# Kernel tuning notes

Measured on AMD Instinct MI355X. Metric: run time of the kernel, lower is better.

The kernel has to match this reference:

```python
import jax, jax.numpy as jnp
import numpy as np

S, B, D = 1024, 32, 1024

def setup_inputs() -> dict:
    key = jax.random.key(0)
    k1, k2, k3, k4, k5 = jax.random.split(key, 5)
    x = jax.random.normal(k1, (S, B, D), dtype=jnp.float32)
    layer_input = jax.random.normal(k2, (S, B, D), dtype=jnp.float32)
    position_embedding = jax.random.normal(k3, (S, B, D), dtype=jnp.float32)
    # pad indicator == 1 (True); random pads, ~half the positions
    encoder_mask = jax.random.randint(k4, (B, S), 0, 2).astype(bool)
    W = jax.random.normal(k5, (D, 1), dtype=jnp.float32) * (1.0 / np.sqrt(D))
    b = jnp.zeros((1,), dtype=jnp.float32)
    return {"x": x, "layer_input": layer_input,
            "position_embedding": position_embedding,
            "encoder_mask": encoder_mask, "W": W, "b": b}

def reference(x, layer_input, position_embedding, encoder_mask, W, b):
    s, bsz, d = x.shape
    valid = (~encoder_mask).astype(x.dtype)            # (B, S)
    sentence_length = valid.sum(axis=-1)               # (B,)
    langtok_index = s - sentence_length                # (B,)
    # predicted soft position in [0, sentence_length]
    pred = jax.nn.sigmoid(x @ W + b)[..., 0]           # (S, B)
    pred = pred * sentence_length[None, :]             # (S, B)
    # absolute positions shifted by language-token offset
    all_pos = jnp.arange(s, dtype=x.dtype)[:, None] - langtok_index[None, :]  # (S, B)
    # distances[i, b, j] = pred[i, b] - all_pos[j, b]
    dist = pred[:, :, None] - all_pos.T[None, :, :]    # (S, B, S)
    prob = 1.0 / (dist * dist + 0.001)                 # reciprocal squared distance
    prob = prob * valid[None, :, :]                    # zero out pads along j
    prob = prob / prob.sum(axis=-1, keepdims=True)     # normalize over source positions
    # weighted sum of position embeddings: (S,B,S) x (S,B,D) -> (S,B,D)
    out = jnp.einsum('ibj,jbd->ibd', prob, position_embedding)
    out = out * valid.T[:, :, None]                    # zero out pad rows
    return out
```

## Files before the change

### kernel.cpp

```cpp
#include <hip/hip_runtime.h>


#define S_ 1024
#define B_ 32
#define D_ 1024

typedef unsigned short us;
typedef __attribute__((ext_vector_type(4))) unsigned short us4;
typedef __attribute__((ext_vector_type(4))) float f4;
typedef __attribute__((ext_vector_type(8))) short short8;

__device__ __forceinline__ float bf2f(us u){
  unsigned v = ((unsigned)u) << 16;
  float f;
  __builtin_memcpy(&f, &v, 4);
  return f;
}
__device__ __forceinline__ us f2bf(float f){
  unsigned v;
  __builtin_memcpy(&v, &f, 4);
  v = v + 0x7fffu + ((v >> 16) & 1u);
  return (us)(v >> 16);
}

__device__ __forceinline__ void gll16(const void* g, void* l){
  __builtin_amdgcn_global_load_lds(
      (const __attribute__((address_space(1))) void*)g,
      (__attribute__((address_space(3))) void*)l,
      16, 0, 0);
}

__global__ __launch_bounds__(256) void prep_k(const unsigned char* __restrict__ mask,
                                              float* __restrict__ valid,
                                              float* __restrict__ slen,
                                              float* __restrict__ ltok)
{
  const int b = blockIdx.x;
  const int t = threadIdx.x;
  __shared__ int flags[5];
  __shared__ int red[256];
  if (t < 5) flags[t] = 0;
  __syncthreads();
  for (int k = 0; k < 32; ++k){
    int p = t * 32 + k;
    unsigned v = mask[p];
    if (v){
      atomicOr(&flags[p & 3], 1);
      if (v > 1u) atomicOr(&flags[4], 1);
    }
  }
  __syncthreads();
  int fmt;
  int any123 = flags[1] | flags[2] | flags[3];
  if (!flags[4]) fmt = any123 ? 0 : 1;
  else           fmt = (flags[0] | flags[1]) ? 2 : 3;

  int cnt = 0;
#pragma unroll
  for (int q = 0; q < 4; ++q){
    int j = t + q * 256;
    size_t idx = (size_t)b * S_ + j;
    unsigned mv;
    if (fmt == 0)      mv = mask[idx];
    else if (fmt == 1) mv = ((const unsigned int*)mask)[idx];
    else if (fmt == 2) mv = ((const unsigned short*)mask)[idx];
    else               mv = ((const unsigned int*)mask)[idx] & 0x7fffffffu;
    valid[idx] = mv ? 0.0f : 1.0f;
    cnt += mv ? 0 : 1;
  }
  red[t] = cnt;
  __syncthreads();
  for (int s = 128; s > 0; s >>= 1){
    if (t < s) red[t] += red[t + s];
    __syncthreads();
  }
  if (t == 0){
    float cn = (float)red[0];
    slen[b] = cn;
    ltok[b] = (float)S_ - cn;
  }
}

__device__ __forceinline__ void rowk_body(int blk, const float* __restrict__ x,
                                          const float* __restrict__ Wp,
                                          const float* __restrict__ bp,
                                          const float* __restrict__ valid,
                                          const float* __restrict__ slen,
                                          const float* __restrict__ ltok,
                                          us* __restrict__ P,
                                          float* __restrict__ rs,
                                          float* __restrict__ c_arr,
                                          bool writeP)
{
  const int wid  = threadIdx.x >> 6;
  const int lane = threadIdx.x & 63;
  const int row  = blk * 4 + wid;
  const int b = row & (B_ - 1);
  const int i = row >> 5;

  const float4* xr = (const float4*)(x + (size_t)row * D_);
  const float4* wr = (const float4*)Wp;
  float acc = 0.f;
#pragma unroll
  for (int q = 0; q < 4; ++q){
    float4 xv = xr[q * 64 + lane];
    float4 wv = wr[q * 64 + lane];
    acc += xv.x * wv.x + xv.y * wv.y + xv.z * wv.z + xv.w * wv.w;
  }
#pragma unroll
  for (int off = 32; off > 0; off >>= 1) acc += __shfl_xor(acc, off);

  float z   = acc + bp[0];
  float sig = 1.f / (1.f + expf(-z));
  float c   = sig * slen[b] + ltok[b];

  const float4* vr = (const float4*)(valid + (size_t)b * S_);
  us4* Pr = (us4*)(P + ((size_t)b * S_ + i) * S_);
  float wsum = 0.f;
#pragma unroll
  for (int q = 0; q < 4; ++q){
    int idx = q * 64 + lane;
    float4 vv = vr[idx];
    float j0 = (float)(idx * 4);
    float d0 = c - j0;
    float d1 = c - (j0 + 1.f);
    float d2 = c - (j0 + 2.f);
    float d3 = c - (j0 + 3.f);
    us p0 = f2bf(vv.x / (d0 * d0 + 1e-3f));
    us p1 = f2bf(vv.y / (d1 * d1 + 1e-3f));
    us p2 = f2bf(vv.z / (d2 * d2 + 1e-3f));
    us p3 = f2bf(vv.w / (d3 * d3 + 1e-3f));
    if (writeP){
      us4 pv; pv.x = p0; pv.y = p1; pv.z = p2; pv.w = p3;
      Pr[idx] = pv;
    }
    wsum += bf2f(p0) + bf2f(p1) + bf2f(p2) + bf2f(p3);
  }
#pragma unroll
  for (int off = 32; off > 0; off >>= 1) wsum += __shfl_xor(wsum, off);

  if (lane == 0){
    float vi = valid[(size_t)b * S_ + i];
    rs[(size_t)b * S_ + i] = (vi != 0.f) ? (vi / wsum) : 0.f;
    c_arr[(size_t)b * S_ + i] = c;
  }
}

__device__ __forceinline__ void transp_body(int j0, int d0, int b,
                                            const float* __restrict__ pe,
                                            us* __restrict__ Etr,
                                            us* tile )
{
  const int t  = threadIdx.x;
  const int rr = t >> 4, cc = t & 15;
#pragma unroll
  for (int q = 0; q < 4; ++q){
    int j = q * 16 + rr;
    float4 v = *(const float4*)(pe + ((size_t)(j0 + j) * B_ + b) * D_ + d0 + cc * 4);
    us4 tv; tv.x = f2bf(v.x); tv.y = f2bf(v.y); tv.z = f2bf(v.z); tv.w = f2bf(v.w);
    *(us4*)&tile[j * 68 + cc * 4] = tv;
  }
  __syncthreads();
#pragma unroll
  for (int q = 0; q < 4; ++q){
    int d = q * 16 + rr;
    us4 v;
    v.x = tile[(cc * 4 + 0) * 68 + d];
    v.y = tile[(cc * 4 + 1) * 68 + d];
    v.z = tile[(cc * 4 + 2) * 68 + d];
    v.w = tile[(cc * 4 + 3) * 68 + d];
    *(us4*)(Etr + ((size_t)b * D_ + d0 + d) * S_ + j0 + cc * 4) = v;
  }
}

__global__ __launch_bounds__(256) void mid_k(const float* __restrict__ x,
                                             const float* __restrict__ Wp,
                                             const float* __restrict__ bp,
                                             const float* __restrict__ valid,
                                             const float* __restrict__ slen,
                                             const float* __restrict__ ltok,
                                             us* __restrict__ P,
                                             float* __restrict__ rs,
                                             float* __restrict__ c_arr,
                                             const float* __restrict__ pe,
                                             us* __restrict__ Etr)
{
  __shared__ us tile[64 * 68];
  const int bid = blockIdx.x;
  if (bid < (S_ * B_ / 4)){
    rowk_body(bid, x, Wp, bp, valid, slen, ltok, P, rs, c_arr, true);
  } else {
    int id2 = bid - (S_ * B_ / 4);
    int jt = id2 & 15;
    int dt = (id2 >> 4) & 15;
    int b  = id2 >> 8;
    transp_body(jt * 64, dt * 64, b, pe, Etr, tile);
  }
}

__global__ __launch_bounds__(512, 2) void gemm_k(const us* __restrict__ P,
                                                 const us* __restrict__ Etr,
                                                 const float* __restrict__ rs,
                                                 float* __restrict__ out)
{
  const int bid = blockIdx.x;
  const int xcd = bid & 7;
  const int s   = bid >> 3;
  const int b   = xcd * 4 + (s >> 4);
  const int t16 = s & 15;
  const int i0  = (t16 >> 2) * 256;
  const int n0  = (t16 & 3) * 256;

  const int tid  = threadIdx.x;
  const int wid  = tid >> 6;
  const int lane = tid & 63;
  const int wm = wid >> 2, wn = wid & 3;
  const int ml = lane & 15, quad = lane >> 4;

  __shared__ __align__(16) us lds[2][4][8192];

  const us* gsrc[4];
  {
    int p = tid;
    int r = p >> 2;
    int c = (p & 3) ^ ((r >> 1) & 3);
    const us* arow = P   + ((size_t)b * S_ + (i0 + r)) * S_;
    const us* brow = Etr + ((size_t)b * D_ + (n0 + r)) * S_;
    gsrc[0] = arow + c * 8;
    gsrc[1] = arow + 32 + c * 8;
    gsrc[2] = brow + c * 8;
    gsrc[3] = brow + 32 + c * 8;
  }
  const int dst0 = wid * 64 * 8;

  int aoff[8], boff[4];
#pragma unroll
  for (int mt = 0; mt < 8; ++mt){
    int r = wm * 128 + mt * 16 + ml;
    aoff[mt] = r * 32 + ((quad ^ ((r >> 1) & 3)) * 8);
  }
#pragma unroll
  for (int nt = 0; nt < 4; ++nt){
    int r = wn * 64 + nt * 16 + ml;
    boff[nt] = r * 32 + ((quad ^ ((r >> 1) & 3)) * 8);
  }

  f4 acc[8][4];
#pragma unroll
  for (int mt = 0; mt < 8; ++mt)
#pragma unroll
    for (int nt = 0; nt < 4; ++nt){
      f4 z = {0.0f, 0.0f, 0.0f, 0.0f};
      acc[mt][nt] = z;
    }

  auto STAGE = [&](int buf, int h, int kt){
    const us* g = gsrc[h] + kt * 64;
    us* l = &lds[buf][h][dst0];
    gll16(g,                 l);
    gll16(g + 128 * S_,      l + 4096);
  };

  STAGE(0, 0, 0); STAGE(0, 2, 0);
  STAGE(0, 1, 0); STAGE(0, 3, 0);
  asm volatile("s_waitcnt vmcnt(4)" ::: "memory");
  __builtin_amdgcn_s_barrier();
  asm volatile("" ::: "memory");

#pragma unroll 1
  for (int kt = 0; kt < 16; ++kt){
    const int buf = kt & 1, nb = buf ^ 1;
    const int ktn = (kt < 15) ? (kt + 1) : 0;
    const us* A0 = lds[buf][0];
    const us* A1 = lds[buf][1];
    const us* B0 = lds[buf][2];
    const us* B1 = lds[buf][3];
    short8 av[4], av2[4], bv[4];

#pragma unroll
    for (int mt = 0; mt < 4; ++mt) av[mt] = *(const short8*)&A0[aoff[mt]];
#pragma unroll
    for (int nt = 0; nt < 4; ++nt) bv[nt] = *(const short8*)&B0[boff[nt]];
    STAGE(nb, 0, ktn);
    __builtin_amdgcn_s_setprio(1);
#pragma unroll
    for (int mt = 0; mt < 4; ++mt)
#pragma unroll
      for (int nt = 0; nt < 4; ++nt)
        acc[mt][nt] = __builtin_amdgcn_mfma_f32_16x16x32_bf16(av[mt], bv[nt], acc[mt][nt], 0, 0, 0);
    __builtin_amdgcn_s_setprio(0);

#pragma unroll
    for (int mt = 0; mt < 4; ++mt) av2[mt] = *(const short8*)&A0[aoff[4 + mt]];
    STAGE(nb, 2, ktn);
    __builtin_amdgcn_s_setprio(1);
#pragma unroll
    for (int mt = 0; mt < 4; ++mt)
#pragma unroll
      for (int nt = 0; nt < 4; ++nt)
        acc[4 + mt][nt] = __builtin_amdgcn_mfma_f32_16x16x32_bf16(av2[mt], bv[nt], acc[4 + mt][nt], 0, 0, 0);
    __builtin_amdgcn_s_setprio(0);

    asm volatile("s_waitcnt vmcnt(4)" ::: "memory");
    __builtin_amdgcn_s_barrier();
    asm volatile("" ::: "memory");

#pragma unroll
    for (int mt = 0; mt < 4; ++mt) av[mt] = *(const short8*)&A1[aoff[mt]];
#pragma unroll
    for (int nt = 0; nt < 4; ++nt) bv[nt] = *(const short8*)&B1[boff[nt]];
    STAGE(nb, 1, ktn);
    __builtin_amdgcn_s_setprio(1);
#pragma unroll
    for (int mt = 0; mt < 4; ++mt)
#pragma unroll
      for (int nt = 0; nt < 4; ++nt)
        acc[mt][nt] = __builtin_amdgcn_mfma_f32_16x16x32_bf16(av[mt], bv[nt], acc[mt][nt], 0, 0, 0);
    __builtin_amdgcn_s_setprio(0);

#pragma unroll
    for (int mt = 0; mt < 4; ++mt) av2[mt] = *(const short8*)&A1[aoff[4 + mt]];
    STAGE(nb, 3, ktn);
    __builtin_amdgcn_s_setprio(1);
#pragma unroll
    for (int mt = 0; mt < 4; ++mt)
#pragma unroll
      for (int nt = 0; nt < 4; ++nt)
        acc[4 + mt][nt] = __builtin_amdgcn_mfma_f32_16x16x32_bf16(av2[mt], bv[nt], acc[4 + mt][nt], 0, 0, 0);
    __builtin_amdgcn_s_setprio(0);

    asm volatile("s_waitcnt vmcnt(4)" ::: "memory");
    __builtin_amdgcn_s_barrier();
    asm volatile("" ::: "memory");
  }
  asm volatile("s_waitcnt vmcnt(0)" ::: "memory");

  const float* rsb = rs + (size_t)b * S_;
#pragma unroll
  for (int mt = 0; mt < 8; ++mt){
#pragma unroll
    for (int reg = 0; reg < 4; ++reg){
      int i = i0 + wm * 128 + mt * 16 + quad * 4 + reg;
      float rv = rsb[i];
      size_t ob = ((size_t)i * B_ + b) * D_;
#pragma unroll
      for (int nt = 0; nt < 4; ++nt){
        int d = n0 + wn * 64 + nt * 16 + ml;
        out[ob + d] = acc[mt][nt][reg] * rv;
      }
    }
  }
}

__global__ __launch_bounds__(256) void rowk_nb(const float* __restrict__ x,
                                               const float* __restrict__ Wp,
                                               const float* __restrict__ bp,
                                               const float* __restrict__ valid,
                                               const float* __restrict__ slen,
                                               const float* __restrict__ ltok,
                                               float* __restrict__ rs,
                                               float* __restrict__ c_arr)
{
  rowk_body(blockIdx.x, x, Wp, bp, valid, slen, ltok, nullptr, rs, c_arr, false);
}

__global__ __launch_bounds__(256) void slow_out_k(const float* __restrict__ pe,
                                                  const float* __restrict__ valid,
                                                  const float* __restrict__ c_arr,
                                                  const float* __restrict__ rs,
                                                  float* __restrict__ out)
{
  const int bid = blockIdx.x;
  const int b = bid & (B_ - 1);
  const int i = bid >> 5;
  const int t = threadIdx.x;
  __shared__ float sw[S_];
  float c  = c_arr[(size_t)b * S_ + i];
  float rv = rs[(size_t)b * S_ + i];
#pragma unroll
  for (int q = 0; q < 4; ++q){
    int j = t + q * 256;
    float d = c - (float)j;
    sw[j] = valid[(size_t)b * S_ + j] / (d * d + 1e-3f);
  }
  __syncthreads();
  float a0 = 0, a1 = 0, a2 = 0, a3 = 0;
  if (rv != 0.0f){
    for (int j = 0; j < S_; ++j){
      float wj = sw[j];
      const float* row = pe + ((size_t)j * B_ + b) * D_;
      a0 += wj * row[t];
      a1 += wj * row[t + 256];
      a2 += wj * row[t + 512];
      a3 += wj * row[t + 768];
    }
  }
  float* orow = out + ((size_t)i * B_ + b) * D_;
  orow[t]       = a0 * rv;
  orow[t + 256] = a1 * rv;
  orow[t + 512] = a2 * rv;
  orow[t + 768] = a3 * rv;
}

extern "C" void kernel_launch(void* const* d_in, const int* in_sizes, int n_in,
                              void* d_out, int out_size, void* d_ws, size_t ws_size,
                              hipStream_t stream)
{
  (void)in_sizes; (void)n_in; (void)out_size;
  const float* x  = (const float*)d_in[0];
  const float* pe = (const float*)d_in[2];
  const unsigned char* mask = (const unsigned char*)d_in[3];
  const float* Wp = (const float*)d_in[4];
  const float* bp = (const float*)d_in[5];
  float* out = (float*)d_out;
  char* ws = (char*)d_ws;

  const size_t offValid = 0;
  const size_t offRs    = offValid + (size_t)B_ * S_ * 4;
  const size_t offSlen  = offRs    + (size_t)B_ * S_ * 4;
  const size_t offLtok  = offSlen  + 128;
  const size_t offC     = offLtok  + 128;
  const size_t offP     = offC     + (size_t)B_ * S_ * 4;
  const size_t offE     = offP     + (size_t)B_ * S_ * S_ * 2;
  const size_t need     = offE     + (size_t)B_ * D_ * S_ * 2;

  float* valid = (float*)(ws + offValid);
  float* rs    = (float*)(ws + offRs);
  float* slen  = (float*)(ws + offSlen);
  float* ltok  = (float*)(ws + offLtok);
  float* c_arr = (float*)(ws + offC);
  us* P   = (us*)(ws + offP);
  us* Etr = (us*)(ws + offE);

  prep_k<<<B_, 256, 0, stream>>>(mask, valid, slen, ltok);
  if (ws_size >= need){
    mid_k<<<16384, 256, 0, stream>>>(x, Wp, bp, valid, slen, ltok, P, rs, c_arr, pe, Etr);
    gemm_k<<<512, 512, 0, stream>>>(P, Etr, rs, out);
  } else {
    rowk_nb<<<S_ * B_ / 4, 256, 0, stream>>>(x, Wp, bp, valid, slen, ltok, rs, c_arr);
    slow_out_k<<<S_ * B_, 256, 0, stream>>>(pe, valid, c_arr, rs, out);
  }
}
```

Measured before the change: 454.6 us.

## Widen transpose tiles with swizzled LDS and interleave transpose and row blocks

```diff
diff --git a/kernel.cpp b/kernel.cpp
--- a/kernel.cpp
+++ b/kernel.cpp
@@ -146,30 +146,36 @@
   }
 }
 
-__device__ __forceinline__ void transp_body(int j0, int d0, int b,
+__device__ __forceinline__ void transp_body(int j0, int dt, int b,
                                             const float* __restrict__ pe,
                                             us* __restrict__ Etr,
                                             us* tile )
 {
-  const int t  = threadIdx.x;
-  const int rr = t >> 4, cc = t & 15;
-#pragma unroll
-  for (int q = 0; q < 4; ++q){
-    int j = q * 16 + rr;
-    float4 v = *(const float4*)(pe + ((size_t)(j0 + j) * B_ + b) * D_ + d0 + cc * 4);
-    us4 tv; tv.x = f2bf(v.x); tv.y = f2bf(v.y); tv.z = f2bf(v.z); tv.w = f2bf(v.w);
-    *(us4*)&tile[j * 68 + cc * 4] = tv;
+  const int t = threadIdx.x;
+  const int w = t >> 6;
+  const int l = t & 63;
+  const int dloc  = (l & 31) * 4;
+  const int jbase = w * 16 + (l >> 5);
+
+#pragma unroll
+  for (int it = 0; it < 8; ++it){
+    int jloc = jbase + it * 2;
+    float4 v = *(const float4*)(pe + ((size_t)(j0 + jloc) * B_ + b) * D_ + dt + dloc);
+    us4 tv; tv[0] = f2bf(v.x); tv[1] = f2bf(v.y); tv[2] = f2bf(v.z); tv[3] = f2bf(v.w);
+    int jc = jloc >> 3, jl = jloc & 7;
+#pragma unroll
+    for (int k = 0; k < 4; ++k){
+      int d = dloc + k;
+      tile[d * 72 + ((jc ^ ((d >> 3) & 7)) << 3) + jl] = tv[k];
+    }
   }
   __syncthreads();
 #pragma unroll
-  for (int q = 0; q < 4; ++q){
-    int d = q * 16 + rr;
-    us4 v;
-    v.x = tile[(cc * 4 + 0) * 68 + d];
-    v.y = tile[(cc * 4 + 1) * 68 + d];
-    v.z = tile[(cc * 4 + 2) * 68 + d];
-    v.w = tile[(cc * 4 + 3) * 68 + d];
-    *(us4*)(Etr + ((size_t)b * D_ + d0 + d) * S_ + j0 + cc * 4) = v;
+  for (int it = 0; it < 4; ++it){
+    int d  = w * 32 + it * 8 + (l >> 3);
+    int jc = l & 7;
+    short8 v = *(const short8*)&tile[d * 72 + ((jc ^ ((d >> 3) & 7)) << 3)];
+    *(short8*)(Etr + ((size_t)b * D_ + dt + d) * S_ + j0 + jc * 8) = v;
   }
 }
 
@@ -185,16 +191,17 @@
                                              const float* __restrict__ pe,
                                              us* __restrict__ Etr)
 {
-  __shared__ us tile[64 * 68];
+  __shared__ us tile[128 * 72];
   const int bid = blockIdx.x;
-  if (bid < (S_ * B_ / 4)){
-    rowk_body(bid, x, Wp, bp, valid, slen, ltok, P, rs, c_arr, true);
+  const int g = bid / 3;
+  const int r = bid - g * 3;
+  if (r){
+    rowk_body(g * 2 + (r - 1), x, Wp, bp, valid, slen, ltok, P, rs, c_arr, true);
   } else {
-    int id2 = bid - (S_ * B_ / 4);
-    int jt = id2 & 15;
-    int dt = (id2 >> 4) & 15;
-    int b  = id2 >> 8;
-    transp_body(jt * 64, dt * 64, b, pe, Etr, tile);
+    int jt  = g & 15;
+    int dt8 = (g >> 4) & 7;
+    int b   = g >> 7;
+    transp_body(jt * 64, dt8 * 128, b, pe, Etr, tile);
   }
 }
 
@@ -434,7 +441,7 @@
 
   prep_k<<<B_, 256, 0, stream>>>(mask, valid, slen, ltok);
   if (ws_size >= need){
-    mid_k<<<16384, 256, 0, stream>>>(x, Wp, bp, valid, slen, ltok, P, rs, c_arr, pe, Etr);
+    mid_k<<<12288, 256, 0, stream>>>(x, Wp, bp, valid, slen, ltok, P, rs, c_arr, pe, Etr);
     gemm_k<<<512, 512, 0, stream>>>(P, Etr, rs, out);
   } else {
     rowk_nb<<<S_ * B_ / 4, 256, 0, stream>>>(x, Wp, bp, valid, slen, ltok, rs, c_arr);
```

Measured after the change: 465.0 us. 1.02x slower.

## Switch GEMM mainloop to 4-slot K=32 ring buffer with three-stage prefetch

Applied to the files above, without the earlier changes.

```diff
diff --git a/kernel.cpp b/kernel.cpp
--- a/kernel.cpp
+++ b/kernel.cpp
@@ -217,19 +217,15 @@
   const int wm = wid >> 2, wn = wid & 3;
   const int ml = lane & 15, quad = lane >> 4;
 
-  __shared__ __align__(16) us lds[2][4][8192];
-
-  const us* gsrc[4];
+  __shared__ __align__(16) us lds[4][2][8192];
+
+  const us* gsrc[2];
   {
     int p = tid;
     int r = p >> 2;
     int c = (p & 3) ^ ((r >> 1) & 3);
-    const us* arow = P   + ((size_t)b * S_ + (i0 + r)) * S_;
-    const us* brow = Etr + ((size_t)b * D_ + (n0 + r)) * S_;
-    gsrc[0] = arow + c * 8;
-    gsrc[1] = arow + 32 + c * 8;
-    gsrc[2] = brow + c * 8;
-    gsrc[3] = brow + 32 + c * 8;
+    gsrc[0] = P   + ((size_t)b * S_ + (i0 + r)) * S_ + c * 8;
+    gsrc[1] = Etr + ((size_t)b * D_ + (n0 + r)) * S_ + c * 8;
   }
   const int dst0 = wid * 64 * 8;
 
@@ -254,34 +250,34 @@
       acc[mt][nt] = z;
     }
 
-  auto STAGE = [&](int buf, int h, int kt){
-    const us* g = gsrc[h] + kt * 64;
-    us* l = &lds[buf][h][dst0];
+  auto STAGE = [&](int slot, int h, int kt){
+    const us* g = gsrc[h] + kt * 32;
+    us* l = &lds[slot][h][dst0];
     gll16(g,                 l);
     gll16(g + 128 * S_,      l + 4096);
   };
 
-  STAGE(0, 0, 0); STAGE(0, 2, 0);
-  STAGE(0, 1, 0); STAGE(0, 3, 0);
-  asm volatile("s_waitcnt vmcnt(4)" ::: "memory");
+  STAGE(0, 0, 0); STAGE(0, 1, 0);
+  STAGE(1, 0, 1); STAGE(1, 1, 1);
+  STAGE(2, 0, 2); STAGE(2, 1, 2);
+  asm volatile("s_waitcnt vmcnt(8)" ::: "memory");
   __builtin_amdgcn_s_barrier();
   asm volatile("" ::: "memory");
 
 #pragma unroll 1
-  for (int kt = 0; kt < 16; ++kt){
-    const int buf = kt & 1, nb = buf ^ 1;
-    const int ktn = (kt < 15) ? (kt + 1) : 0;
-    const us* A0 = lds[buf][0];
-    const us* A1 = lds[buf][1];
-    const us* B0 = lds[buf][2];
-    const us* B1 = lds[buf][3];
+  for (int kt = 0; kt < 32; ++kt){
+    const int sl  = kt & 3;
+    const int st  = (kt + 3) & 3;
+    const int ktn = (kt < 29) ? (kt + 3) : 31;
+    const us* A = lds[sl][0];
+    const us* B = lds[sl][1];
     short8 av[4], av2[4], bv[4];
 
 #pragma unroll
-    for (int mt = 0; mt < 4; ++mt) av[mt] = *(const short8*)&A0[aoff[mt]];
-#pragma unroll
-    for (int nt = 0; nt < 4; ++nt) bv[nt] = *(const short8*)&B0[boff[nt]];
-    STAGE(nb, 0, ktn);
+    for (int mt = 0; mt < 4; ++mt) av[mt] = *(const short8*)&A[aoff[mt]];
+#pragma unroll
+    for (int nt = 0; nt < 4; ++nt) bv[nt] = *(const short8*)&B[boff[nt]];
+    STAGE(st, 0, ktn);
     __builtin_amdgcn_s_setprio(1);
 #pragma unroll
     for (int mt = 0; mt < 4; ++mt)
@@ -291,8 +287,8 @@
     __builtin_amdgcn_s_setprio(0);
 
 #pragma unroll
-    for (int mt = 0; mt < 4; ++mt) av2[mt] = *(const short8*)&A0[aoff[4 + mt]];
-    STAGE(nb, 2, ktn);
+    for (int mt = 0; mt < 4; ++mt) av2[mt] = *(const short8*)&A[aoff[4 + mt]];
+    STAGE(st, 1, ktn);
     __builtin_amdgcn_s_setprio(1);
 #pragma unroll
     for (int mt = 0; mt < 4; ++mt)
@@ -301,35 +297,7 @@
         acc[4 + mt][nt] = __builtin_amdgcn_mfma_f32_16x16x32_bf16(av2[mt], bv[nt], acc[4 + mt][nt], 0, 0, 0);
     __builtin_amdgcn_s_setprio(0);
 
-    asm volatile("s_waitcnt vmcnt(4)" ::: "memory");
-    __builtin_amdgcn_s_barrier();
-    asm volatile("" ::: "memory");
-
-#pragma unroll
-    for (int mt = 0; mt < 4; ++mt) av[mt] = *(const short8*)&A1[aoff[mt]];
-#pragma unroll
-    for (int nt = 0; nt < 4; ++nt) bv[nt] = *(const short8*)&B1[boff[nt]];
-    STAGE(nb, 1, ktn);
-    __builtin_amdgcn_s_setprio(1);
-#pragma unroll
-    for (int mt = 0; mt < 4; ++mt)
-#pragma unroll
-      for (int nt = 0; nt < 4; ++nt)
-        acc[mt][nt] = __builtin_amdgcn_mfma_f32_16x16x32_bf16(av[mt], bv[nt], acc[mt][nt], 0, 0, 0);
-    __builtin_amdgcn_s_setprio(0);
-
-#pragma unroll
-    for (int mt = 0; mt < 4; ++mt) av2[mt] = *(const short8*)&A1[aoff[4 + mt]];
-    STAGE(nb, 3, ktn);
-    __builtin_amdgcn_s_setprio(1);
-#pragma unroll
-    for (int mt = 0; mt < 4; ++mt)
-#pragma unroll
-      for (int nt = 0; nt < 4; ++nt)
-        acc[4 + mt][nt] = __builtin_amdgcn_mfma_f32_16x16x32_bf16(av2[mt], bv[nt], acc[4 + mt][nt], 0, 0, 0);
-    __builtin_amdgcn_s_setprio(0);
-
-    asm volatile("s_waitcnt vmcnt(4)" ::: "memory");
+    asm volatile("s_waitcnt vmcnt(8)" ::: "memory");
     __builtin_amdgcn_s_barrier();
     asm volatile("" ::: "memory");
   }
```

Measured after the change: 454.5 us. About the same (-0.0%).
